# Optimization experiments

Measured on AMD Instinct MI355X. Metric: run time of the kernel, lower is better.

## Reference

```python
import jax, jax.numpy as jnp
import numpy as np

HIDDEN = 256
HEADS = 4
HEAD_DIM = HIDDEN // HEADS
SCALE = HEAD_DIM ** -0.5
N1, N2 = 6000, 6000


def setup_inputs() -> dict:
    key = jax.random.key(0)
    ks = jax.random.split(key, 12)
    s = 1.0 / np.sqrt(HIDDEN)
    return {
        "kg1_emb": jax.random.normal(ks[0], (N1, HIDDEN), jnp.float32),
        "kg2_emb": jax.random.normal(ks[1], (N2, HIDDEN), jnp.float32),
        "alignment_matrix": jax.random.bernoulli(ks[2], 0.01, (N1, N2)).astype(jnp.float32),
        "Wq": jax.random.normal(ks[3], (HIDDEN, HIDDEN), jnp.float32) * s,
        "bq": jnp.zeros((HIDDEN,), jnp.float32),
        "Wk": jax.random.normal(ks[4], (HIDDEN, HIDDEN), jnp.float32) * s,
        "bk": jnp.zeros((HIDDEN,), jnp.float32),
        "Wv": jax.random.normal(ks[5], (HIDDEN, HIDDEN), jnp.float32) * s,
        "bv": jnp.zeros((HIDDEN,), jnp.float32),
        "Wo": jax.random.normal(ks[6], (HIDDEN, HIDDEN), jnp.float32) * s,
        "bo": jnp.zeros((HIDDEN,), jnp.float32),
    }


def _cross_attend(q_emb, kv_emb, align, Wq, bq, Wk, bk, Wv, bv):
    # q_emb: [Nq, H*D], kv_emb: [Nk, H*D], align: [Nq, Nk]
    Nq, Nk = q_emb.shape[0], kv_emb.shape[0]
    Q = (q_emb @ Wq.T + bq).reshape(Nq, HEADS, HEAD_DIM)
    K = (kv_emb @ Wk.T + bk).reshape(Nk, HEADS, HEAD_DIM)
    V = (kv_emb @ Wv.T + bv).reshape(Nk, HEADS, HEAD_DIM)
    # einsum('nih,mjh->nmij').mean(-1) == Q against head-mean of K (same math)
    Kbar = K.mean(axis=1)  # [Nk, D]
    scores = jnp.einsum('nid,md->nmi', Q, Kbar) * SCALE  # [Nq, Nk, HEADS]
    scores = scores * align[:, :, None]                  # multiplicative mask
    w = jax.nn.softmax(scores, axis=1)                   # over kv entities
    out = jnp.einsum('nmh,mhd->nhd', w, V)               # [Nq, HEADS, D]
    return out.reshape(Nq, HIDDEN)


def reference(kg1_emb, kg2_emb, alignment_matrix, Wq, bq, Wk, bk, Wv, bv, Wo, bo):
    kg1_from_kg2 = _cross_attend(kg1_emb, kg2_emb, alignment_matrix,
                                 Wq, bq, Wk, bk, Wv, bv)
    kg1_enhanced = kg1_emb + (kg1_from_kg2 @ Wo.T + bo)
    kg2_from_kg1 = _cross_attend(kg2_emb, kg1_emb, alignment_matrix.T,
                                 Wq, bq, Wk, bk, Wv, bv)
    kg2_enhanced = kg2_emb + (kg2_from_kg1 @ Wo.T + bo)
    return (kg1_enhanced, kg2_enhanced)
```

## Files before the change

kernel.cpp:

```cpp
#include <hip/hip_runtime.h>
#include <hip/hip_bf16.h>
#include <stdint.h>

typedef __bf16 bf16_t;
typedef __bf16 bf16x8 __attribute__((ext_vector_type(8)));
typedef __bf16 bf16x4 __attribute__((ext_vector_type(4)));
typedef float f32x4 __attribute__((ext_vector_type(4)));

#define NROW 6000
#define HID 256
#define NHEAD 4
#define HD 64
#define ATT_SCALE 0.125f
#define MTOT 12000
#define CAP 128
#define NCH16 2250000

#define SCAN_BLOCKS  ((NCH16 + 255) / 256)
#define PROJ_BLOCKS  (188 * 12)
#define CSC_BLOCKS   ((NROW * CAP) / 256)
#define WSTR 264

__global__ __launch_bounds__(256)
void k1_proj_scan(const float* __restrict__ e1, const float* __restrict__ e2,
                  const float* __restrict__ wq, const float* __restrict__ wk,
                  const float* __restrict__ wv,
                  const float* __restrict__ bq, const float* __restrict__ bk,
                  const float* __restrict__ bv,
                  bf16_t* __restrict__ Q, bf16_t* __restrict__ Kf, bf16_t* __restrict__ V,
                  const float* __restrict__ am,
                  int* __restrict__ rcur,
                  int* __restrict__ csr)
{
    __shared__ bf16_t lds_w[64 * WSTR];

    if (blockIdx.x < PROJ_BLOCKS) {
        int bx   = blockIdx.x;
        int m0   = (bx % 188) * 64;
        int n0   = (bx / 188) * 64;
        int wave = threadIdx.x >> 6;
        int lane = threadIdx.x & 63;
        int r16  = lane & 15;
        int quad = lane >> 4;

        int sel = n0 >> 8;
        int jb  = n0 & 255;
        const float* wsrc = (sel == 0) ? wq : (sel == 1) ? wk : wv;
        const float* bias = (sel == 0) ? bq : (sel == 1) ? bk : bv;

        for (int i = threadIdx.x; i < 64 * 64; i += 256) {
            int row = i >> 6;
            int kq  = (i & 63) * 4;
            f32x4 w4 = *(const f32x4*)(wsrc + (size_t)(jb + row) * HID + kq);
            bf16x4 b4;
#pragma unroll
            for (int z = 0; z < 4; ++z) b4[z] = (bf16_t)w4[z];
            *(bf16x4*)(&lds_w[row * WSTR + kq]) = b4;
        }
        __syncthreads();

        int arow = m0 + wave * 16 + r16;
        int rr   = arow < MTOT ? arow : MTOT - 1;
        const float* asrc = (rr < NROW) ? (e1 + (size_t)rr * HID)
                                        : (e2 + (size_t)(rr - NROW) * HID);

        f32x4 acc0 = {0,0,0,0}, acc1 = {0,0,0,0}, acc2 = {0,0,0,0}, acc3 = {0,0,0,0};
#pragma unroll
        for (int kk = 0; kk < HID; kk += 32) {
            f32x4 af0 = *(const f32x4*)(asrc + kk + quad * 8);
            f32x4 af1 = *(const f32x4*)(asrc + kk + quad * 8 + 4);
            bf16x8 a;
#pragma unroll
            for (int i = 0; i < 4; ++i) { a[i] = (bf16_t)af0[i]; a[4 + i] = (bf16_t)af1[i]; }
            const bf16_t* b0 = lds_w + (size_t)r16 * WSTR + kk + quad * 8;
            bf16x8 f0 = *(const bf16x8*)(b0);
            bf16x8 f1 = *(const bf16x8*)(b0 + 16 * WSTR);
            bf16x8 f2 = *(const bf16x8*)(b0 + 32 * WSTR);
            bf16x8 f3 = *(const bf16x8*)(b0 + 48 * WSTR);
            acc0 = __builtin_amdgcn_mfma_f32_16x16x32_bf16(a, f0, acc0, 0, 0, 0);
            acc1 = __builtin_amdgcn_mfma_f32_16x16x32_bf16(a, f1, acc1, 0, 0, 0);
            acc2 = __builtin_amdgcn_mfma_f32_16x16x32_bf16(a, f2, acc2, 0, 0, 0);
            acc3 = __builtin_amdgcn_mfma_f32_16x16x32_bf16(a, f3, acc3, 0, 0, 0);
        }
        f32x4 accs[4] = {acc0, acc1, acc2, acc3};
        bf16_t* dst = (sel == 0) ? Q : (sel == 1) ? Kf : V;
        int rbase = m0 + wave * 16 + quad * 4;
#pragma unroll
        for (int nt = 0; nt < 4; ++nt) {
            int j = jb + nt * 16 + r16;
            float bb = bias[j];
#pragma unroll
            for (int rg = 0; rg < 4; ++rg) {
                int r = rbase + rg;
                if (r < MTOT)
                    dst[(size_t)r * HID + j] = (bf16_t)(accs[nt][rg] + bb);
            }
        }
        return;
    }

    int lane = threadIdx.x & 63;
    int ch   = (blockIdx.x - PROJ_BLOCKS) * 256 + threadIdx.x;
    bool oob = (ch >= NCH16);
    int che  = oob ? (NCH16 - 1) : ch;

    unsigned int nzmask = 0;
    if (!oob) {
        const uint4* p4 = (const uint4*)((const unsigned int*)am + (size_t)che * 16);
        uint4 u0 = p4[0], u1 = p4[1], u2 = p4[2], u3 = p4[3];
        unsigned int any = u0.x | u0.y | u0.z | u0.w | u1.x | u1.y | u1.z | u1.w
                         | u2.x | u2.y | u2.z | u2.w | u3.x | u3.y | u3.z | u3.w;
        if (any) {
            unsigned int w[16] = {u0.x, u0.y, u0.z, u0.w, u1.x, u1.y, u1.z, u1.w,
                                  u2.x, u2.y, u2.z, u2.w, u3.x, u3.y, u3.z, u3.w};
#pragma unroll
            for (int p = 0; p < 16; ++p)
                if (w[p]) nzmask |= 1u << p;
        }
    }
    int n  = che / 375;
    int m0 = (che - n * 375) * 16;
    int c  = __popc(nzmask);

    int p = c;
#pragma unroll
    for (int off = 1; off < 64; off <<= 1) {
        int t = __shfl_up(p, off);
        if (lane >= off) p += t;
    }
    int excl  = p - c;
    int total = __shfl(p, 63);

    int nFirst = __shfl(n, 0);
    int nLast  = __shfl(n, 63);
    unsigned long long mb = __ballot(n == nLast);
    int s0  = __ffsll(mb) - 1;
    int pS0 = __shfl(excl, s0);

    int baseB = 0;
    if (lane == s0) {
        int totalB = total - pS0;
        if (totalB > 0) baseB = atomicAdd(rcur + nLast, totalB);
    }
    baseB = __shfl(baseB, s0);
    int baseA = 0;
    if (s0 > 0) {
        if (lane == 0 && pS0 > 0) baseA = atomicAdd(rcur + nFirst, pS0);
        baseA = __shfl(baseA, 0);
    }

    int myOff = (n == nLast) ? (baseB + excl - pS0) : (baseA + excl);
    if (c) {
        int* dst = csr + (size_t)n * CAP;
        int w = 0;
#pragma unroll
        for (int pb = 0; pb < 16; ++pb) {
            if (nzmask & (1u << pb)) {
                int idx = myOff + (w++);
                if (idx < CAP) dst[idx] = m0 + pb;
            }
        }
    }
}

__global__ __launch_bounds__(256)
void k2_aux(const bf16_t* __restrict__ Kf, const bf16_t* __restrict__ V,
            bf16_t* __restrict__ Kbar, float* __restrict__ Vsum,
            const int* __restrict__ rcnt, const int* __restrict__ csr,
            int* __restrict__ ccur, int* __restrict__ csc)
{
    int b = blockIdx.x;
    if (b < 3000) {
        int id = b * 256 + threadIdx.x;
        int m = id >> 6, d = id & 63;
        const bf16_t* kr = Kf + (size_t)m * HID + d;
        Kbar[id] = (bf16_t)(0.25f * ((float)kr[0] + (float)kr[64] +
                                     (float)kr[128] + (float)kr[192]));
    } else if (b < 3048) {
        int idx = b - 3000;
        int g = idx / 24;
        int seg = idx - g * 24;
        int j = threadIdx.x;
        const bf16_t* base = V + ((size_t)(g * NROW + seg * 250)) * HID + j;
        float s = 0.f;
        for (int m = 0; m < 250; ++m) s += (float)base[(size_t)m * HID];
        atomicAdd(Vsum + g * HID + j, s);
    } else {
        int tid = (b - 3048) * 256 + threadIdx.x;
        int n = tid >> 7, j = tid & (CAP - 1);
        if (n >= NROW) return;
        int cnt = rcnt[n]; if (cnt > CAP) cnt = CAP;
        if (j >= cnt) return;
        int m = csr[(size_t)n * CAP + j];
        int slot = atomicAdd(ccur + m, 1);
        if (slot < CAP) csc[(size_t)m * CAP + slot] = n;
    }
}

__global__ __launch_bounds__(256)
void attn_kernel(const bf16_t* __restrict__ Q, const bf16_t* __restrict__ Kbar,
                 const bf16_t* __restrict__ V, const float* __restrict__ Vsum,
                 const int* __restrict__ rcnt, const int* __restrict__ ccnt,
                 const int* __restrict__ csr, const int* __restrict__ csc,
                 bf16_t* __restrict__ att)
{
    __shared__ __align__(16) bf16_t qsb[HID];
    __shared__ int   ml[CAP];
    __shared__ float sc[CAP * 5];
    __shared__ float w0s[NHEAD];
    __shared__ float red[4 * HID];

    int dir = blockIdx.y;
    int n   = blockIdx.x;
    int t   = threadIdx.x;
    int wave = t >> 6, lane = t & 63;

    size_t qrow = (size_t)(dir ? NROW + n : n);
    const bf16_t* kb_base = Kbar + (dir ? 0 : (size_t)NROW * HD);
    const bf16_t* v_base  = V    + (dir ? 0 : (size_t)NROW * HID);
    const float*  vs      = Vsum + (dir ? 0 : HID);
    const int*    lst     = (dir ? csc : csr) + (size_t)n * CAP;
    int cnt = (dir ? ccnt : rcnt)[n];
    if (cnt > CAP) cnt = CAP;

    qsb[t] = Q[qrow * HID + t];
    for (int j = t; j < cnt; j += 256) ml[j] = lst[j];
    __syncthreads();

    int m16  = lane & 15;
    int quad = lane >> 4;

    {
        bf16x8 b0, b1;
        if (m16 < NHEAD) {
            b0 = *(const bf16x8*)(qsb + m16 * HD + 0  + quad * 8);
            b1 = *(const bf16x8*)(qsb + m16 * HD + 32 + quad * 8);
        } else {
            b0 = (bf16x8)(bf16_t)0.f;
            b1 = (bf16x8)(bf16_t)0.f;
        }
        for (int jt = wave; jt * 16 < cnt; jt += 4) {
            int j  = jt * 16 + m16;
            int jj = j < cnt ? j : cnt - 1;
            int row = ml[jj];
            const bf16_t* ap = kb_base + (size_t)row * HD + quad * 8;
            bf16x8 a0 = *(const bf16x8*)(ap);
            bf16x8 a1 = *(const bf16x8*)(ap + 32);
            f32x4 acc = {0, 0, 0, 0};
            acc = __builtin_amdgcn_mfma_f32_16x16x32_bf16(a0, b0, acc, 0, 0, 0);
            acc = __builtin_amdgcn_mfma_f32_16x16x32_bf16(a1, b1, acc, 0, 0, 0);
            if (m16 < NHEAD) {
#pragma unroll
                for (int rg = 0; rg < 4; ++rg) {
                    int jw = jt * 16 + quad * 4 + rg;
                    if (jw < cnt) sc[jw * 5 + m16] = acc[rg] * ATT_SCALE;
                }
            }
        }
    }
    __syncthreads();

    {
        int head = wave;
        float M = 0.0f;
        for (int j = lane; j < cnt; j += 64) M = fmaxf(M, sc[j * 5 + head]);
        for (int off = 32; off; off >>= 1) M = fmaxf(M, __shfl_xor(M, off));
        float e0 = __expf(-M);
        float e[2]; int k = 0;
        float S = 0.f;
        for (int j = lane; j < cnt; j += 64, ++k) { e[k] = __expf(sc[j * 5 + head] - M); S += e[k]; }
        for (int off = 32; off; off >>= 1) S += __shfl_xor(S, off);
        float Z = S + (float)(NROW - cnt) * e0;
        float invZ = 1.0f / Z;
        k = 0;
        for (int j = lane; j < cnt; j += 64, ++k) sc[j * 5 + head] = (e[k] - e0) * invZ;
        if (lane == 0) w0s[head] = e0 * invZ;
    }
    __syncthreads();

    int h3 = lane >> 4;
    int dq = lane & 15;
    int colb = h3 * HD + dq * 4;
    float a0 = 0.f, a1 = 0.f, a2 = 0.f, a3 = 0.f;
    {
        int j = wave;
        for (; j + 12 < cnt; j += 16) {
            int   m0 = ml[j];            int   m1 = ml[j + 4];
            int   m2 = ml[j + 8];        int   m3 = ml[j + 12];
            float c0 = sc[j * 5 + h3];   float c1 = sc[(j + 4) * 5 + h3];
            float c2 = sc[(j + 8) * 5 + h3]; float c3 = sc[(j + 12) * 5 + h3];
            bf16x4 r0 = *(const bf16x4*)(v_base + (size_t)m0 * HID + colb);
            bf16x4 r1 = *(const bf16x4*)(v_base + (size_t)m1 * HID + colb);
            bf16x4 r2 = *(const bf16x4*)(v_base + (size_t)m2 * HID + colb);
            bf16x4 r3 = *(const bf16x4*)(v_base + (size_t)m3 * HID + colb);
            a0 += c0 * (float)r0[0] + c1 * (float)r1[0] + c2 * (float)r2[0] + c3 * (float)r3[0];
            a1 += c0 * (float)r0[1] + c1 * (float)r1[1] + c2 * (float)r2[1] + c3 * (float)r3[1];
            a2 += c0 * (float)r0[2] + c1 * (float)r1[2] + c2 * (float)r2[2] + c3 * (float)r3[2];
            a3 += c0 * (float)r0[3] + c1 * (float)r1[3] + c2 * (float)r2[3] + c3 * (float)r3[3];
        }
        for (; j < cnt; j += 4) {
            int   m0 = ml[j];
            float c0 = sc[j * 5 + h3];
            bf16x4 r0 = *(const bf16x4*)(v_base + (size_t)m0 * HID + colb);
            a0 += c0 * (float)r0[0];
            a1 += c0 * (float)r0[1];
            a2 += c0 * (float)r0[2];
            a3 += c0 * (float)r0[3];
        }
    }
    red[wave * 256 + colb + 0] = a0;
    red[wave * 256 + colb + 1] = a1;
    red[wave * 256 + colb + 2] = a2;
    red[wave * 256 + colb + 3] = a3;
    __syncthreads();
    float tot = red[t] + red[256 + t] + red[512 + t] + red[768 + t]
              + w0s[t >> 6] * vs[t];
    att[qrow * HID + t] = (bf16_t)tot;
}

__global__ __launch_bounds__(256)
void proj_out_kernel(const bf16_t* __restrict__ att, const float* __restrict__ wo,
                     const float* __restrict__ bo,
                     const float* __restrict__ e1, const float* __restrict__ e2,
                     float* __restrict__ out)
{
    __shared__ bf16_t lds_w[64 * WSTR];

    int m0   = blockIdx.x * 64;
    int n0   = blockIdx.y * 64;
    int wave = threadIdx.x >> 6;
    int lane = threadIdx.x & 63;
    int r16  = lane & 15;
    int quad = lane >> 4;

    for (int i = threadIdx.x; i < 64 * 64; i += 256) {
        int row = i >> 6;
        int kq  = (i & 63) * 4;
        f32x4 w4 = *(const f32x4*)(wo + (size_t)(n0 + row) * HID + kq);
        bf16x4 b4;
#pragma unroll
        for (int z = 0; z < 4; ++z) b4[z] = (bf16_t)w4[z];
        *(bf16x4*)(&lds_w[row * WSTR + kq]) = b4;
    }
    __syncthreads();

    int arow = m0 + wave * 16 + r16;
    int rr   = arow < MTOT ? arow : MTOT - 1;
    const bf16_t* asrc = att + (size_t)rr * HID;

    f32x4 acc0 = {0,0,0,0}, acc1 = {0,0,0,0}, acc2 = {0,0,0,0}, acc3 = {0,0,0,0};
#pragma unroll
    for (int kk = 0; kk < HID; kk += 32) {
        bf16x8 a = *(const bf16x8*)(asrc + kk + quad * 8);
        const bf16_t* b0 = lds_w + (size_t)r16 * WSTR + kk + quad * 8;
        bf16x8 f0 = *(const bf16x8*)(b0);
        bf16x8 f1 = *(const bf16x8*)(b0 + 16 * WSTR);
        bf16x8 f2 = *(const bf16x8*)(b0 + 32 * WSTR);
        bf16x8 f3 = *(const bf16x8*)(b0 + 48 * WSTR);
        acc0 = __builtin_amdgcn_mfma_f32_16x16x32_bf16(a, f0, acc0, 0, 0, 0);
        acc1 = __builtin_amdgcn_mfma_f32_16x16x32_bf16(a, f1, acc1, 0, 0, 0);
        acc2 = __builtin_amdgcn_mfma_f32_16x16x32_bf16(a, f2, acc2, 0, 0, 0);
        acc3 = __builtin_amdgcn_mfma_f32_16x16x32_bf16(a, f3, acc3, 0, 0, 0);
    }
    f32x4 accs[4] = {acc0, acc1, acc2, acc3};
    int rbase = m0 + wave * 16 + quad * 4;
#pragma unroll
    for (int nt = 0; nt < 4; ++nt) {
        int j = n0 + nt * 16 + r16;
        float bb = bo[j];
#pragma unroll
        for (int rg = 0; rg < 4; ++rg) {
            int r = rbase + rg;
            if (r < MTOT) {
                const float* emb = (r < NROW) ? (e1 + (size_t)r * HID)
                                              : (e2 + (size_t)(r - NROW) * HID);
                float v = accs[nt][rg] + bb + emb[j];
                out[(size_t)r * HID + j] = v;
            }
        }
    }
}

extern "C" void kernel_launch(void* const* d_in, const int* in_sizes, int n_in,
                              void* d_out, int out_size, void* d_ws, size_t ws_size,
                              hipStream_t stream)
{
    const float* e1 = (const float*)d_in[0];
    const float* e2 = (const float*)d_in[1];
    const float* am = (const float*)d_in[2];
    const float* wq = (const float*)d_in[3];
    const float* bq = (const float*)d_in[4];
    const float* wk = (const float*)d_in[5];
    const float* bk = (const float*)d_in[6];
    const float* wv = (const float*)d_in[7];
    const float* bv = (const float*)d_in[8];
    const float* wo = (const float*)d_in[9];
    const float* bo = (const float*)d_in[10];
    float* out = (float*)d_out;

    size_t off = 0;
    char* base = (char*)d_ws;
    auto alloc = [&](size_t bytes) -> void* {
        void* p = base + off;
        off += (bytes + 255) & ~(size_t)255;
        return p;
    };
    bf16_t* Q    = (bf16_t*)alloc((size_t)MTOT * HID * 2);
    bf16_t* Kf   = (bf16_t*)alloc((size_t)MTOT * HID * 2);
    bf16_t* V    = (bf16_t*)alloc((size_t)MTOT * HID * 2);
    bf16_t* Kbar = (bf16_t*)alloc((size_t)MTOT * HD * 2);
    bf16_t* att  = (bf16_t*)alloc((size_t)MTOT * HID * 2);
    int*    csr  = (int*)   alloc((size_t)NROW * CAP * 4);
    int*    csc  = (int*)   alloc((size_t)NROW * CAP * 4);
    int*    rcur = (int*)   alloc(NROW * 4);
    int*    ccur = (int*)   alloc(NROW * 4);
    float*  Vsum = (float*) alloc(2 * HID * 4);

    size_t zero_bytes = (size_t)((char*)Vsum - (char*)rcur) + 2 * HID * 4;
    hipMemsetAsync(rcur, 0, zero_bytes, stream);

    k1_proj_scan<<<PROJ_BLOCKS + SCAN_BLOCKS, 256, 0, stream>>>(
        e1, e2, wq, wk, wv, bq, bk, bv, Q, Kf, V, am, rcur, csr);

    k2_aux<<<6048, 256, 0, stream>>>(Kf, V, Kbar, Vsum, rcur, csr, ccur, csc);

    attn_kernel<<<dim3(NROW, 2), 256, 0, stream>>>(
        Q, Kbar, V, Vsum, rcur, ccur, csr, csc, att);

    proj_out_kernel<<<dim3(188, 4), 256, 0, stream>>>(att, wo, bo, e1, e2, out);
}
```

Before: 356.2 us.

## Scan alignment rows per wave without atomics, fold memset into kernel, drop LDS weight staging

The alignment scan now gives each wave one full row and builds that row's CSR list with in-wave prefix sums. This removes the global atomics and the cross-row split logic, and writes the row counts directly. The separate memset is replaced by zeroing blocks inside the first kernel, which saves one launch. Both projection GEMMs now read fp32 weights straight from global memory and convert them in registers instead of staging them in LDS, trading shared-memory traffic and a barrier for redundant global and L2 weight reads.

```diff
diff --git a/kernel.cpp b/kernel.cpp
--- a/kernel.cpp
+++ b/kernel.cpp
@@ -14,151 +14,139 @@
 #define ATT_SCALE 0.125f
 #define MTOT 12000
 #define CAP 128
-#define NCH16 2250000
-
-#define SCAN_BLOCKS  ((NCH16 + 255) / 256)
-#define PROJ_BLOCKS  (188 * 12)
-#define CSC_BLOCKS   ((NROW * CAP) / 256)
-#define WSTR 264
+
+#define SCANB 1500
+#define ZEROB 26
+#define PROJB (188 * 12)
+
+__device__ inline bf16x8 cvt8(const float* __restrict__ p)
+{
+    f32x4 x0 = *(const f32x4*)p;
+    f32x4 x1 = *(const f32x4*)(p + 4);
+    bf16x8 r;
+#pragma unroll
+    for (int i = 0; i < 4; ++i) { r[i] = (bf16_t)x0[i]; r[4 + i] = (bf16_t)x1[i]; }
+    return r;
+}
 
 __global__ __launch_bounds__(256)
-void k1_proj_scan(const float* __restrict__ e1, const float* __restrict__ e2,
+void k1_scan_proj(const float* __restrict__ am,
+                  int* __restrict__ rcnt, int* __restrict__ csr,
+                  int* __restrict__ zbase,
+                  const float* __restrict__ e1, const float* __restrict__ e2,
                   const float* __restrict__ wq, const float* __restrict__ wk,
                   const float* __restrict__ wv,
                   const float* __restrict__ bq, const float* __restrict__ bk,
                   const float* __restrict__ bv,
-                  bf16_t* __restrict__ Q, bf16_t* __restrict__ Kf, bf16_t* __restrict__ V,
-                  const float* __restrict__ am,
-                  int* __restrict__ rcur,
-                  int* __restrict__ csr)
-{
-    __shared__ bf16_t lds_w[64 * WSTR];
-
-    if (blockIdx.x < PROJ_BLOCKS) {
-        int bx   = blockIdx.x;
-        int m0   = (bx % 188) * 64;
-        int n0   = (bx / 188) * 64;
-        int wave = threadIdx.x >> 6;
-        int lane = threadIdx.x & 63;
-        int r16  = lane & 15;
-        int quad = lane >> 4;
-
-        int sel = n0 >> 8;
-        int jb  = n0 & 255;
-        const float* wsrc = (sel == 0) ? wq : (sel == 1) ? wk : wv;
-        const float* bias = (sel == 0) ? bq : (sel == 1) ? bk : bv;
-
-        for (int i = threadIdx.x; i < 64 * 64; i += 256) {
-            int row = i >> 6;
-            int kq  = (i & 63) * 4;
-            f32x4 w4 = *(const f32x4*)(wsrc + (size_t)(jb + row) * HID + kq);
-            bf16x4 b4;
-#pragma unroll
-            for (int z = 0; z < 4; ++z) b4[z] = (bf16_t)w4[z];
-            *(bf16x4*)(&lds_w[row * WSTR + kq]) = b4;
-        }
-        __syncthreads();
-
-        int arow = m0 + wave * 16 + r16;
-        int rr   = arow < MTOT ? arow : MTOT - 1;
-        const float* asrc = (rr < NROW) ? (e1 + (size_t)rr * HID)
-                                        : (e2 + (size_t)(rr - NROW) * HID);
-
-        f32x4 acc0 = {0,0,0,0}, acc1 = {0,0,0,0}, acc2 = {0,0,0,0}, acc3 = {0,0,0,0};
-#pragma unroll
-        for (int kk = 0; kk < HID; kk += 32) {
-            f32x4 af0 = *(const f32x4*)(asrc + kk + quad * 8);
-            f32x4 af1 = *(const f32x4*)(asrc + kk + quad * 8 + 4);
-            bf16x8 a;
-#pragma unroll
-            for (int i = 0; i < 4; ++i) { a[i] = (bf16_t)af0[i]; a[4 + i] = (bf16_t)af1[i]; }
-            const bf16_t* b0 = lds_w + (size_t)r16 * WSTR + kk + quad * 8;
-            bf16x8 f0 = *(const bf16x8*)(b0);
-            bf16x8 f1 = *(const bf16x8*)(b0 + 16 * WSTR);
-            bf16x8 f2 = *(const bf16x8*)(b0 + 32 * WSTR);
-            bf16x8 f3 = *(const bf16x8*)(b0 + 48 * WSTR);
-            acc0 = __builtin_amdgcn_mfma_f32_16x16x32_bf16(a, f0, acc0, 0, 0, 0);
-            acc1 = __builtin_amdgcn_mfma_f32_16x16x32_bf16(a, f1, acc1, 0, 0, 0);
-            acc2 = __builtin_amdgcn_mfma_f32_16x16x32_bf16(a, f2, acc2, 0, 0, 0);
-            acc3 = __builtin_amdgcn_mfma_f32_16x16x32_bf16(a, f3, acc3, 0, 0, 0);
-        }
-        f32x4 accs[4] = {acc0, acc1, acc2, acc3};
-        bf16_t* dst = (sel == 0) ? Q : (sel == 1) ? Kf : V;
-        int rbase = m0 + wave * 16 + quad * 4;
-#pragma unroll
-        for (int nt = 0; nt < 4; ++nt) {
-            int j = jb + nt * 16 + r16;
-            float bb = bias[j];
-#pragma unroll
-            for (int rg = 0; rg < 4; ++rg) {
-                int r = rbase + rg;
-                if (r < MTOT)
-                    dst[(size_t)r * HID + j] = (bf16_t)(accs[nt][rg] + bb);
+                  bf16_t* __restrict__ Q, bf16_t* __restrict__ Kf, bf16_t* __restrict__ V)
+{
+    int lane = threadIdx.x & 63;
+    int wave = threadIdx.x >> 6;
+
+    if (blockIdx.x < SCANB) {
+        int n = blockIdx.x * 4 + wave;
+        const uint4* rowp = (const uint4*)(am + (size_t)n * NROW);
+
+        unsigned int masks[6];
+#pragma unroll
+        for (int i = 0; i < 6; ++i) {
+            int c = i * 64 + lane;
+            unsigned int m = 0;
+            if (c < 375) {
+                const uint4* p4 = rowp + c * 4;
+                uint4 u0 = p4[0], u1 = p4[1], u2 = p4[2], u3 = p4[3];
+                unsigned int any = u0.x | u0.y | u0.z | u0.w | u1.x | u1.y | u1.z | u1.w
+                                 | u2.x | u2.y | u2.z | u2.w | u3.x | u3.y | u3.z | u3.w;
+                if (any) {
+                    unsigned int w[16] = {u0.x, u0.y, u0.z, u0.w, u1.x, u1.y, u1.z, u1.w,
+                                          u2.x, u2.y, u2.z, u2.w, u3.x, u3.y, u3.z, u3.w};
+#pragma unroll
+                    for (int p = 0; p < 16; ++p)
+                        if (w[p]) m |= 1u << p;
+                }
             }
-        }
+            masks[i] = m;
+        }
+
+        int* dst = csr + (size_t)n * CAP;
+        int base = 0;
+#pragma unroll
+        for (int i = 0; i < 6; ++i) {
+            unsigned int m = masks[i];
+            int c = __popc(m);
+            int p = c;
+#pragma unroll
+            for (int off = 1; off < 64; off <<= 1) {
+                int t = __shfl_up(p, off);
+                if (lane >= off) p += t;
+            }
+            int excl  = p - c;
+            int total = __shfl(p, 63);
+            if (m) {
+                int col0 = (i * 64 + lane) * 16;
+                int w = 0;
+#pragma unroll
+                for (int pb = 0; pb < 16; ++pb) {
+                    if (m & (1u << pb)) {
+                        int idx = base + excl + (w++);
+                        if (idx < CAP) dst[idx] = col0 + pb;
+                    }
+                }
+            }
+            base += total;
+        }
+        if (lane == 0) rcnt[n] = base;
         return;
     }
 
-    int lane = threadIdx.x & 63;
-    int ch   = (blockIdx.x - PROJ_BLOCKS) * 256 + threadIdx.x;
-    bool oob = (ch >= NCH16);
-    int che  = oob ? (NCH16 - 1) : ch;
-
-    unsigned int nzmask = 0;
-    if (!oob) {
-        const uint4* p4 = (const uint4*)((const unsigned int*)am + (size_t)che * 16);
-        uint4 u0 = p4[0], u1 = p4[1], u2 = p4[2], u3 = p4[3];
-        unsigned int any = u0.x | u0.y | u0.z | u0.w | u1.x | u1.y | u1.z | u1.w
-                         | u2.x | u2.y | u2.z | u2.w | u3.x | u3.y | u3.z | u3.w;
-        if (any) {
-            unsigned int w[16] = {u0.x, u0.y, u0.z, u0.w, u1.x, u1.y, u1.z, u1.w,
-                                  u2.x, u2.y, u2.z, u2.w, u3.x, u3.y, u3.z, u3.w};
-#pragma unroll
-            for (int p = 0; p < 16; ++p)
-                if (w[p]) nzmask |= 1u << p;
-        }
-    }
-    int n  = che / 375;
-    int m0 = (che - n * 375) * 16;
-    int c  = __popc(nzmask);
-
-    int p = c;
-#pragma unroll
-    for (int off = 1; off < 64; off <<= 1) {
-        int t = __shfl_up(p, off);
-        if (lane >= off) p += t;
-    }
-    int excl  = p - c;
-    int total = __shfl(p, 63);
-
-    int nFirst = __shfl(n, 0);
-    int nLast  = __shfl(n, 63);
-    unsigned long long mb = __ballot(n == nLast);
-    int s0  = __ffsll(mb) - 1;
-    int pS0 = __shfl(excl, s0);
-
-    int baseB = 0;
-    if (lane == s0) {
-        int totalB = total - pS0;
-        if (totalB > 0) baseB = atomicAdd(rcur + nLast, totalB);
-    }
-    baseB = __shfl(baseB, s0);
-    int baseA = 0;
-    if (s0 > 0) {
-        if (lane == 0 && pS0 > 0) baseA = atomicAdd(rcur + nFirst, pS0);
-        baseA = __shfl(baseA, 0);
-    }
-
-    int myOff = (n == nLast) ? (baseB + excl - pS0) : (baseA + excl);
-    if (c) {
-        int* dst = csr + (size_t)n * CAP;
-        int w = 0;
-#pragma unroll
-        for (int pb = 0; pb < 16; ++pb) {
-            if (nzmask & (1u << pb)) {
-                int idx = myOff + (w++);
-                if (idx < CAP) dst[idx] = m0 + pb;
-            }
+    if (blockIdx.x < SCANB + ZEROB) {
+        int i = (blockIdx.x - SCANB) * 256 + threadIdx.x;
+        if (i < NROW + 2 * HID) zbase[i] = 0;
+        return;
+    }
+
+    int bx   = blockIdx.x - (SCANB + ZEROB);
+    int m0   = (bx % 188) * 64;
+    int n0   = (bx / 188) * 64;
+    int r16  = lane & 15;
+    int quad = lane >> 4;
+
+    int sel = n0 >> 8;
+    int jb  = n0 & 255;
+    const float* wsrc = (sel == 0) ? wq : (sel == 1) ? wk : wv;
+    const float* bias = (sel == 0) ? bq : (sel == 1) ? bk : bv;
+
+    int arow = m0 + wave * 16 + r16;
+    int rr   = arow < MTOT ? arow : MTOT - 1;
+    const float* asrc = (rr < NROW) ? (e1 + (size_t)rr * HID)
+                                    : (e2 + (size_t)(rr - NROW) * HID);
+
+    f32x4 acc0 = {0,0,0,0}, acc1 = {0,0,0,0}, acc2 = {0,0,0,0}, acc3 = {0,0,0,0};
+#pragma unroll
+    for (int kk = 0; kk < HID; kk += 32) {
+        bf16x8 a = cvt8(asrc + kk + quad * 8);
+        const float* b0 = wsrc + (size_t)(jb + r16) * HID + kk + quad * 8;
+        bf16x8 f0 = cvt8(b0);
+        bf16x8 f1 = cvt8(b0 + 16 * HID);
+        bf16x8 f2 = cvt8(b0 + 32 * HID);
+        bf16x8 f3 = cvt8(b0 + 48 * HID);
+        acc0 = __builtin_amdgcn_mfma_f32_16x16x32_bf16(a, f0, acc0, 0, 0, 0);
+        acc1 = __builtin_amdgcn_mfma_f32_16x16x32_bf16(a, f1, acc1, 0, 0, 0);
+        acc2 = __builtin_amdgcn_mfma_f32_16x16x32_bf16(a, f2, acc2, 0, 0, 0);
+        acc3 = __builtin_amdgcn_mfma_f32_16x16x32_bf16(a, f3, acc3, 0, 0, 0);
+    }
+    f32x4 accs[4] = {acc0, acc1, acc2, acc3};
+    bf16_t* dst = (sel == 0) ? Q : (sel == 1) ? Kf : V;
+    int rbase = m0 + wave * 16 + quad * 4;
+#pragma unroll
+    for (int nt = 0; nt < 4; ++nt) {
+        int j = jb + nt * 16 + r16;
+        float bb = bias[j];
+#pragma unroll
+        for (int rg = 0; rg < 4; ++rg) {
+            int r = rbase + rg;
+            if (r < MTOT)
+                dst[(size_t)r * HID + j] = (bf16_t)(accs[nt][rg] + bb);
         }
     }
 }
@@ -324,8 +312,6 @@
                      const float* __restrict__ e1, const float* __restrict__ e2,
                      float* __restrict__ out)
 {
-    __shared__ bf16_t lds_w[64 * WSTR];
-
     int m0   = blockIdx.x * 64;
     int n0   = blockIdx.y * 64;
     int wave = threadIdx.x >> 6;
@@ -333,17 +319,6 @@
     int r16  = lane & 15;
     int quad = lane >> 4;
 
-    for (int i = threadIdx.x; i < 64 * 64; i += 256) {
-        int row = i >> 6;
-        int kq  = (i & 63) * 4;
-        f32x4 w4 = *(const f32x4*)(wo + (size_t)(n0 + row) * HID + kq);
-        bf16x4 b4;
-#pragma unroll
-        for (int z = 0; z < 4; ++z) b4[z] = (bf16_t)w4[z];
-        *(bf16x4*)(&lds_w[row * WSTR + kq]) = b4;
-    }
-    __syncthreads();
-
     int arow = m0 + wave * 16 + r16;
     int rr   = arow < MTOT ? arow : MTOT - 1;
     const bf16_t* asrc = att + (size_t)rr * HID;
@@ -352,11 +327,11 @@
 #pragma unroll
     for (int kk = 0; kk < HID; kk += 32) {
         bf16x8 a = *(const bf16x8*)(asrc + kk + quad * 8);
-        const bf16_t* b0 = lds_w + (size_t)r16 * WSTR + kk + quad * 8;
-        bf16x8 f0 = *(const bf16x8*)(b0);
-        bf16x8 f1 = *(const bf16x8*)(b0 + 16 * WSTR);
-        bf16x8 f2 = *(const bf16x8*)(b0 + 32 * WSTR);
-        bf16x8 f3 = *(const bf16x8*)(b0 + 48 * WSTR);
+        const float* b0 = wo + (size_t)(n0 + r16) * HID + kk + quad * 8;
+        bf16x8 f0 = cvt8(b0);
+        bf16x8 f1 = cvt8(b0 + 16 * HID);
+        bf16x8 f2 = cvt8(b0 + 32 * HID);
+        bf16x8 f3 = cvt8(b0 + 48 * HID);
         acc0 = __builtin_amdgcn_mfma_f32_16x16x32_bf16(a, f0, acc0, 0, 0, 0);
         acc1 = __builtin_amdgcn_mfma_f32_16x16x32_bf16(a, f1, acc1, 0, 0, 0);
         acc2 = __builtin_amdgcn_mfma_f32_16x16x32_bf16(a, f2, acc2, 0, 0, 0);
@@ -412,20 +387,17 @@
     bf16_t* att  = (bf16_t*)alloc((size_t)MTOT * HID * 2);
     int*    csr  = (int*)   alloc((size_t)NROW * CAP * 4);
     int*    csc  = (int*)   alloc((size_t)NROW * CAP * 4);
-    int*    rcur = (int*)   alloc(NROW * 4);
+    int*    rcnt = (int*)   alloc(NROW * 4);
     int*    ccur = (int*)   alloc(NROW * 4);
     float*  Vsum = (float*) alloc(2 * HID * 4);
 
-    size_t zero_bytes = (size_t)((char*)Vsum - (char*)rcur) + 2 * HID * 4;
-    hipMemsetAsync(rcur, 0, zero_bytes, stream);
-
-    k1_proj_scan<<<PROJ_BLOCKS + SCAN_BLOCKS, 256, 0, stream>>>(
-        e1, e2, wq, wk, wv, bq, bk, bv, Q, Kf, V, am, rcur, csr);
-
-    k2_aux<<<6048, 256, 0, stream>>>(Kf, V, Kbar, Vsum, rcur, csr, ccur, csc);
+    k1_scan_proj<<<SCANB + ZEROB + PROJB, 256, 0, stream>>>(
+        am, rcnt, csr, ccur, e1, e2, wq, wk, wv, bq, bk, bv, Q, Kf, V);
+
+    k2_aux<<<6048, 256, 0, stream>>>(Kf, V, Kbar, Vsum, rcnt, csr, ccur, csc);
 
     attn_kernel<<<dim3(NROW, 2), 256, 0, stream>>>(
-        Q, Kbar, V, Vsum, rcur, ccur, csr, csc, att);
+        Q, Kbar, V, Vsum, rcnt, ccur, csr, csc, att);
 
     proj_out_kernel<<<dim3(188, 4), 256, 0, stream>>>(att, wo, bo, e1, e2, out);
 }
```

Measured after the change: 420.8 us. 18.1% more time.

## Halve projection LDS weight tile and preload A fragments into registers

Applied to the files above, without the earlier changes.

The projection path now loads and converts all eight A-operand fragments into registers before staging weights. The 64-row weight tile is staged in two 32-row halves through a half-size LDS buffer, with an extra barrier between halves. This is meant to cut LDS use per block, which could raise occupancy for the fused kernel, and to issue the global A loads early so they overlap the weight staging. In exchange it adds more VGPR pressure, extra syncs and a second global weight load pass.

```diff
diff --git a/kernel.cpp b/kernel.cpp
--- a/kernel.cpp
+++ b/kernel.cpp
@@ -18,8 +18,17 @@
 
 #define SCAN_BLOCKS  ((NCH16 + 255) / 256)
 #define PROJ_BLOCKS  (188 * 12)
-#define CSC_BLOCKS   ((NROW * CAP) / 256)
 #define WSTR 264
+
+__device__ inline bf16x8 cvt8(const float* __restrict__ p)
+{
+    f32x4 x0 = *(const f32x4*)p;
+    f32x4 x1 = *(const f32x4*)(p + 4);
+    bf16x8 r;
+#pragma unroll
+    for (int i = 0; i < 4; ++i) { r[i] = (bf16_t)x0[i]; r[4 + i] = (bf16_t)x1[i]; }
+    return r;
+}
 
 __global__ __launch_bounds__(256)
 void k1_proj_scan(const float* __restrict__ e1, const float* __restrict__ e2,
@@ -32,7 +41,7 @@
                   int* __restrict__ rcur,
                   int* __restrict__ csr)
 {
-    __shared__ bf16_t lds_w[64 * WSTR];
+    __shared__ bf16_t lds_w[32 * WSTR];
 
     if (blockIdx.x < PROJ_BLOCKS) {
         int bx   = blockIdx.x;
@@ -48,7 +57,19 @@
         const float* wsrc = (sel == 0) ? wq : (sel == 1) ? wk : wv;
         const float* bias = (sel == 0) ? bq : (sel == 1) ? bk : bv;
 
-        for (int i = threadIdx.x; i < 64 * 64; i += 256) {
+        int arow = m0 + wave * 16 + r16;
+        int rr   = arow < MTOT ? arow : MTOT - 1;
+        const float* asrc = (rr < NROW) ? (e1 + (size_t)rr * HID)
+                                        : (e2 + (size_t)(rr - NROW) * HID);
+
+        bf16x8 afr[8];
+#pragma unroll
+        for (int k8 = 0; k8 < 8; ++k8)
+            afr[k8] = cvt8(asrc + k8 * 32 + quad * 8);
+
+        f32x4 acc0 = {0,0,0,0}, acc1 = {0,0,0,0}, acc2 = {0,0,0,0}, acc3 = {0,0,0,0};
+
+        for (int i = threadIdx.x; i < 32 * 64; i += 256) {
             int row = i >> 6;
             int kq  = (i & 63) * 4;
             f32x4 w4 = *(const f32x4*)(wsrc + (size_t)(jb + row) * HID + kq);
@@ -58,30 +79,35 @@
             *(bf16x4*)(&lds_w[row * WSTR + kq]) = b4;
         }
         __syncthreads();
-
-        int arow = m0 + wave * 16 + r16;
-        int rr   = arow < MTOT ? arow : MTOT - 1;
-        const float* asrc = (rr < NROW) ? (e1 + (size_t)rr * HID)
-                                        : (e2 + (size_t)(rr - NROW) * HID);
-
-        f32x4 acc0 = {0,0,0,0}, acc1 = {0,0,0,0}, acc2 = {0,0,0,0}, acc3 = {0,0,0,0};
-#pragma unroll
-        for (int kk = 0; kk < HID; kk += 32) {
-            f32x4 af0 = *(const f32x4*)(asrc + kk + quad * 8);
-            f32x4 af1 = *(const f32x4*)(asrc + kk + quad * 8 + 4);
-            bf16x8 a;
-#pragma unroll
-            for (int i = 0; i < 4; ++i) { a[i] = (bf16_t)af0[i]; a[4 + i] = (bf16_t)af1[i]; }
-            const bf16_t* b0 = lds_w + (size_t)r16 * WSTR + kk + quad * 8;
+#pragma unroll
+        for (int k8 = 0; k8 < 8; ++k8) {
+            const bf16_t* b0 = lds_w + (size_t)r16 * WSTR + k8 * 32 + quad * 8;
             bf16x8 f0 = *(const bf16x8*)(b0);
             bf16x8 f1 = *(const bf16x8*)(b0 + 16 * WSTR);
-            bf16x8 f2 = *(const bf16x8*)(b0 + 32 * WSTR);
-            bf16x8 f3 = *(const bf16x8*)(b0 + 48 * WSTR);
-            acc0 = __builtin_amdgcn_mfma_f32_16x16x32_bf16(a, f0, acc0, 0, 0, 0);
-            acc1 = __builtin_amdgcn_mfma_f32_16x16x32_bf16(a, f1, acc1, 0, 0, 0);
-            acc2 = __builtin_amdgcn_mfma_f32_16x16x32_bf16(a, f2, acc2, 0, 0, 0);
-            acc3 = __builtin_amdgcn_mfma_f32_16x16x32_bf16(a, f3, acc3, 0, 0, 0);
-        }
+            acc0 = __builtin_amdgcn_mfma_f32_16x16x32_bf16(afr[k8], f0, acc0, 0, 0, 0);
+            acc1 = __builtin_amdgcn_mfma_f32_16x16x32_bf16(afr[k8], f1, acc1, 0, 0, 0);
+        }
+        __syncthreads();
+
+        for (int i = threadIdx.x; i < 32 * 64; i += 256) {
+            int row = i >> 6;
+            int kq  = (i & 63) * 4;
+            f32x4 w4 = *(const f32x4*)(wsrc + (size_t)(jb + 32 + row) * HID + kq);
+            bf16x4 b4;
+#pragma unroll
+            for (int z = 0; z < 4; ++z) b4[z] = (bf16_t)w4[z];
+            *(bf16x4*)(&lds_w[row * WSTR + kq]) = b4;
+        }
+        __syncthreads();
+#pragma unroll
+        for (int k8 = 0; k8 < 8; ++k8) {
+            const bf16_t* b0 = lds_w + (size_t)r16 * WSTR + k8 * 32 + quad * 8;
+            bf16x8 f2 = *(const bf16x8*)(b0);
+            bf16x8 f3 = *(const bf16x8*)(b0 + 16 * WSTR);
+            acc2 = __builtin_amdgcn_mfma_f32_16x16x32_bf16(afr[k8], f2, acc2, 0, 0, 0);
+            acc3 = __builtin_amdgcn_mfma_f32_16x16x32_bf16(afr[k8], f3, acc3, 0, 0, 0);
+        }
+
         f32x4 accs[4] = {acc0, acc1, acc2, acc3};
         bf16_t* dst = (sel == 0) ? Q : (sel == 1) ? Kf : V;
         int rbase = m0 + wave * 16 + quad * 4;
```

New measurement: 355.1 us. About the same (-0.3%).
